# Kernel optimization log

Hardware: AMD Instinct MI355X
Metric: run time of the kernel (lower is better)

## Reference

```python
import jax, jax.numpy as jnp
import numpy as np

EPS = 1e-5  # BatchNorm2d default eps


def _conv3x3(x, w):
    # x: [B,C,H,W], w: [O,I,3,3], stride 1, 'same' padding (autopad k=3 -> p=1)
    return jax.lax.conv_general_dilated(
        x, w, window_strides=(1, 1), padding=((1, 1), (1, 1)),
        dimension_numbers=("NCHW", "OIHW", "NCHW"))


def _bn(x, g, b, m, v):
    # inference-mode BatchNorm2d with materialized running stats
    scale = (g / jnp.sqrt(v + EPS))[None, :, None, None]
    return (x - m[None, :, None, None]) * scale + b[None, :, None, None]


def _silu(x):
    return x * jax.nn.sigmoid(x)


def _pam(y, q_w, q_b, k_w, k_b, v_w, v_b, pam_gamma):
    # PAM_Module: full pixel-wise self-attention over N = H*W tokens
    B, C, H, W = y.shape
    N = H * W
    yf = y.reshape(B, C, N)
    # 1x1 convs expressed as channel matmuls; q_w: [C//8, C], v_w: [C, C]
    q = jnp.einsum("oc,bcn->bno", q_w, yf) + q_b                 # [B, N, C//8]
    k = jnp.einsum("oc,bcn->bon", k_w, yf) + k_b[None, :, None]  # [B, C//8, N]
    v = jnp.einsum("oc,bcn->bon", v_w, yf) + v_b[None, :, None]  # [B, C, N]
    energy = jnp.einsum("bno,bom->bnm", q, k)                    # [B, N, N]
    attn = jax.nn.softmax(energy, axis=-1)
    # torch: bmm(v, attn.permute(0,2,1)) -> out[b,c,n] = sum_m v[b,c,m] * attn[b,n,m]
    out = jnp.einsum("bcm,bnm->bcn", v, attn).reshape(B, C, H, W)
    return pam_gamma * out + y


def setup_inputs() -> dict:
    key = jax.random.key(0)
    ks = jax.random.split(key, 16)
    B, C1, C2, H, W = 4, 64, 64, 64, 64
    C_ = C2 // 2          # e = 0.5
    C8 = C2 // 8          # PAM q/k channels
    s = 0.05
    inp = {
        "x": jax.random.normal(ks[0], (B, C1, H, W), jnp.float32),
        # cv1: Conv(c1, c_, 3, 1)
        "cv1_w": jax.random.normal(ks[1], (C_, C1, 3, 3), jnp.float32) * s,
        "bn1_g": jax.random.uniform(ks[2], (C_,), jnp.float32, 0.5, 1.5),
        "bn1_b": jax.random.normal(ks[3], (C_,), jnp.float32) * s,
        "bn1_m": jax.random.normal(ks[4], (C_,), jnp.float32) * s,
        "bn1_v": jax.random.uniform(ks[5], (C_,), jnp.float32, 0.5, 1.5),
        # cv2: Conv(c_, c2, 3, 1)
        "cv2_w": jax.random.normal(ks[6], (C2, C_, 3, 3), jnp.float32) * s,
        "bn2_g": jax.random.uniform(ks[7], (C2,), jnp.float32, 0.5, 1.5),
        "bn2_b": jax.random.normal(ks[8], (C2,), jnp.float32) * s,
        "bn2_m": jax.random.normal(ks[9], (C2,), jnp.float32) * s,
        "bn2_v": jax.random.uniform(ks[10], (C2,), jnp.float32, 0.5, 1.5),
        # PAM 1x1 convs (flattened kernels) + biases + gamma
        "q_w": jax.random.normal(ks[11], (C8, C2), jnp.float32) * s,
        "q_b": jax.random.normal(ks[12], (C8,), jnp.float32) * s,
        "k_w": jax.random.normal(ks[13], (C8, C2), jnp.float32) * s,
        "k_b": jax.random.normal(ks[14], (C8,), jnp.float32) * s,
        "v_w": jax.random.normal(ks[15], (C2, C2), jnp.float32) * s,
        "v_b": jnp.zeros((C2,), jnp.float32),
        "pam_gamma": jnp.float32(0.5),  # torch inits 0 (identity); nonzero to exercise path
    }
    return inp


def reference(x, cv1_w, bn1_g, bn1_b, bn1_m, bn1_v,
              cv2_w, bn2_g, bn2_b, bn2_m, bn2_v,
              q_w, q_b, k_w, k_b, v_w, v_b, pam_gamma):
    y = _silu(_bn(_conv3x3(x, cv1_w), bn1_g, bn1_b, bn1_m, bn1_v))   # cv1
    y = _silu(_bn(_conv3x3(y, cv2_w), bn2_g, bn2_b, bn2_m, bn2_v))   # cv2
    # SAA: PAM applied twice on identical input and summed == 2 * PAM(y)
    att = 2.0 * _pam(y, q_w, q_b, k_w, k_b, v_w, v_b, pam_gamma)
    return x + att  # shortcut active (c1 == c2)
```

## Files before the change

### kernel.cpp

```cpp
#include <hip/hip_runtime.h>
#include <hip/hip_bf16.h>

#define NB 4
#define NN 4096

typedef short  bf16x8 __attribute__((ext_vector_type(8)));
typedef float  f32x4  __attribute__((ext_vector_type(4)));

static __device__ __forceinline__ ushort f2bf(float f) {
    unsigned u = __float_as_uint(f);
    u += 0x7fffu + ((u >> 16) & 1u);
    return (ushort)(u >> 16);
}

__global__ __launch_bounds__(256) void prep(
    const float* __restrict__ x, const float* __restrict__ w1, const float* __restrict__ w2,
    ushort* __restrict__ xt, ushort* __restrict__ W1r, ushort* __restrict__ W2r)
{
    const int tid = threadIdx.x;
    const int blk = blockIdx.x;
    if (blk < 256) {
        __shared__ float Ts[64][66];
        const int b = blk >> 6, n0 = (blk & 63) * 64;
        const int wv = tid >> 6, lane = tid & 63;
        #pragma unroll
        for (int i = 0; i < 16; ++i) {
            int ci = i * 4 + wv, nn = lane;
            Ts[ci][nn] = x[((size_t)b * 64 + ci) * NN + n0 + nn];
        }
        __syncthreads();
        #pragma unroll
        for (int i = 0; i < 16; ++i) {
            int nn = i * 4 + wv, ci = lane;
            xt[((size_t)b * NN + n0 + nn) * 64 + ci] = f2bf(Ts[ci][nn]);
        }
    } else if (blk < 258) {
        const int base = (blk - 256) * 9216;
        #pragma unroll
        for (int i = 0; i < 36; ++i) {
            int e = base + i * 256 + tid;
            int co = e / 576, k = e % 576, tap = k >> 6, ci = k & 63;
            W1r[e] = f2bf(w1[((size_t)co * 64 + ci) * 9 + tap]);
        }
    } else {
        const int base = (blk - 258) * 9216;
        #pragma unroll
        for (int i = 0; i < 36; ++i) {
            int e = base + i * 256 + tid;
            int co = e / 288, k = e % 288, tap = k >> 5, ci = k & 31;
            W2r[e] = f2bf(w2[((size_t)co * 32 + ci) * 9 + tap]);
        }
    }
}

__global__ __launch_bounds__(256) void conv1_mfma(
    const ushort* __restrict__ xt, const ushort* __restrict__ W1r,
    const float* __restrict__ bng, const float* __restrict__ bnb,
    const float* __restrict__ bnm, const float* __restrict__ bnv,
    ushort* __restrict__ y1t)
{
    __shared__ __align__(16) ushort As[32 * 600];
    __shared__ __align__(16) ushort Xs[24 * 66 * 8];

    const int tid = threadIdx.x;
    const int h = blockIdx.x, b = blockIdx.y;

    #pragma unroll
    for (int i = 0; i < 9; ++i) {
        int cid = i * 256 + tid;
        int row = cid / 72, off = cid % 72;
        *(uint4*)&As[row * 600 + off * 8] = *(const uint4*)(W1r + (size_t)cid * 8);
    }
    #pragma unroll
    for (int r = 0; r < 3; ++r) {
        int gh = h - 1 + r;
        #pragma unroll
        for (int i = 0; i < 2; ++i) {
            int cid = i * 256 + tid;
            int w_ = cid >> 3, cc = cid & 7;
            uint4 v = {0, 0, 0, 0};
            if ((unsigned)gh < 64u)
                v = *(const uint4*)(xt + ((size_t)(b * NN + gh * 64) * 64) + (size_t)cid * 8);
            *(uint4*)&Xs[((r * 8 + cc) * 66 + (w_ + 1)) * 8] = v;
        }
    }
    if (tid < 48) {
        int r = tid >> 4, q = tid & 15, cc = q >> 1, side = (q & 1) * 65;
        uint4 z = {0, 0, 0, 0};
        *(uint4*)&Xs[((r * 8 + cc) * 66 + side) * 8] = z;
    }
    __syncthreads();

    const int lane = tid & 63, wv = tid >> 6;
    const int quad = lane >> 4, l15 = lane & 15;
    const int ch = wv & 1, ph = wv >> 1;

    f32x4 acc[2] = {{0.f,0.f,0.f,0.f},{0.f,0.f,0.f,0.f}};
    #pragma unroll
    for (int kk = 0; kk < 18; ++kk) {
        const int tap = kk >> 1;
        const int dyr = tap / 3, dx = tap % 3;
        bf16x8 af = *(const bf16x8*)&As[(ch * 16 + l15) * 600 + kk * 32 + quad * 8];
        #pragma unroll
        for (int s = 0; s < 2; ++s) {
            int p = ph * 32 + s * 16 + l15;
            bf16x8 bf = *(const bf16x8*)&Xs[((dyr * 8 + (kk & 1) * 4 + quad) * 66 + p + dx) * 8];
            acc[s] = __builtin_amdgcn_mfma_f32_16x16x32_bf16(af, bf, acc[s], 0, 0, 0);
        }
    }

    const int cb = ch * 16 + quad * 4;
    float sc[4], bs[4];
    #pragma unroll
    for (int r = 0; r < 4; ++r) {
        int co = cb + r;
        sc[r] = bng[co] / sqrtf(bnv[co] + 1e-5f);
        bs[r] = bnb[co] - bnm[co] * sc[r];
    }
    #pragma unroll
    for (int s = 0; s < 2; ++s) {
        int p = ph * 32 + s * 16 + l15;
        ushort u4[4];
        #pragma unroll
        for (int r = 0; r < 4; ++r) {
            float pre = acc[s][r] * sc[r] + bs[r];
            u4[r] = f2bf(pre / (1.f + __expf(-pre)));
        }
        *(uint2*)&y1t[((size_t)(b * NN + h * 64 + p)) * 32 + cb] = *(uint2*)u4;
    }
}

__global__ __launch_bounds__(256) void conv2qkv(
    const ushort* __restrict__ y1t, const ushort* __restrict__ W2r,
    const float* __restrict__ bng, const float* __restrict__ bnb,
    const float* __restrict__ bnm, const float* __restrict__ bnv,
    const float* __restrict__ qw, const float* __restrict__ qb,
    const float* __restrict__ kw, const float* __restrict__ kb,
    const float* __restrict__ vw, const float* __restrict__ vb,
    float* __restrict__ y, ushort* __restrict__ q8,
    ushort* __restrict__ ko, ushort* __restrict__ vt)
{
    __shared__ __align__(16) ushort As[64 * 312];
    __shared__ __align__(16) ushort Xs[12 * 66 * 8];
    __shared__ __align__(16) ushort Yt[64 * 76];
    __shared__ __align__(16) ushort Wq[80 * 76];
    __shared__ float Bv[80];

    const int tid = threadIdx.x;
    const int h = blockIdx.x, b = blockIdx.y;

    #pragma unroll
    for (int i = 0; i < 9; ++i) {
        int cid = i * 256 + tid;
        int row = cid / 36, off = cid % 36;
        *(uint4*)&As[row * 312 + off * 8] = *(const uint4*)(W2r + (size_t)cid * 8);
    }
    #pragma unroll
    for (int r = 0; r < 3; ++r) {
        int gh = h - 1 + r;
        int cid = tid;
        int w_ = cid >> 2, cc = cid & 3;
        uint4 v = {0, 0, 0, 0};
        if ((unsigned)gh < 64u)
            v = *(const uint4*)(y1t + ((size_t)(b * NN + gh * 64) * 32) + (size_t)cid * 8);
        *(uint4*)&Xs[((r * 4 + cc) * 66 + (w_ + 1)) * 8] = v;
    }
    if (tid < 24) {
        int r = tid >> 3, q = tid & 7, cc = q >> 1, side = (q & 1) * 65;
        uint4 z = {0, 0, 0, 0};
        *(uint4*)&Xs[((r * 4 + cc) * 66 + side) * 8] = z;
    }
    for (int i = tid; i < 2560; i += 256) {
        int chw = i >> 5, c2 = (i & 31) * 2;
        const float* src = (chw < 8) ? (qw + chw * 64 + c2)
                         : (chw < 16) ? (kw + (chw - 8) * 64 + c2)
                         : (vw + (chw - 16) * 64 + c2);
        float2 v2 = *(const float2*)src;
        *(unsigned*)&Wq[chw * 76 + c2] = ((unsigned)f2bf(v2.y) << 16) | f2bf(v2.x);
    }
    if (tid < 80) Bv[tid] = (tid < 8) ? qb[tid] : (tid < 16) ? kb[tid - 8] : vb[tid - 16];
    __syncthreads();

    const int lane = tid & 63, wv = tid >> 6;
    const int quad = lane >> 4, l15 = lane & 15;

    f32x4 acc[4] = {{0.f,0.f,0.f,0.f},{0.f,0.f,0.f,0.f},{0.f,0.f,0.f,0.f},{0.f,0.f,0.f,0.f}};
    #pragma unroll
    for (int kk = 0; kk < 9; ++kk) {
        const int dyr = kk / 3, dx = kk % 3;
        bf16x8 af = *(const bf16x8*)&As[(wv * 16 + l15) * 312 + kk * 32 + quad * 8];
        #pragma unroll
        for (int s = 0; s < 4; ++s) {
            int p = s * 16 + l15;
            bf16x8 bf = *(const bf16x8*)&Xs[((dyr * 4 + quad) * 66 + p + dx) * 8];
            acc[s] = __builtin_amdgcn_mfma_f32_16x16x32_bf16(af, bf, acc[s], 0, 0, 0);
        }
    }

    const int cb = wv * 16 + quad * 4;
    float sc[4], bs[4];
    #pragma unroll
    for (int r = 0; r < 4; ++r) {
        int co = cb + r;
        sc[r] = bng[co] / sqrtf(bnv[co] + 1e-5f);
        bs[r] = bnb[co] - bnm[co] * sc[r];
    }
    #pragma unroll
    for (int s = 0; s < 4; ++s) {
        int p = s * 16 + l15;
        #pragma unroll
        for (int r = 0; r < 4; ++r) {
            float pre = acc[s][r] * sc[r] + bs[r];
            float res = pre / (1.f + __expf(-pre));
            y[((size_t)(b * 64 + cb + r)) * NN + h * 64 + p] = res;
            Yt[p * 76 + cb + r] = f2bf(res);
        }
    }
    __syncthreads();

    bf16x8 aY0 = *(const bf16x8*)&Yt[(wv * 16 + l15) * 76 + quad * 8];
    bf16x8 aY1 = *(const bf16x8*)&Yt[(wv * 16 + l15) * 76 + 32 + quad * 8];
    const int nbase = h * 64 + wv * 16 + quad * 4;
    const int vtile = h * 2 + (wv >> 1);
    const int vslot = quad * 8 + (wv & 1) * 4;
    #pragma unroll
    for (int cht = 0; cht < 5; ++cht) {
        bf16x8 bW0 = *(const bf16x8*)&Wq[(cht * 16 + l15) * 76 + quad * 8];
        bf16x8 bW1 = *(const bf16x8*)&Wq[(cht * 16 + l15) * 76 + 32 + quad * 8];
        f32x4 qa = {0.f, 0.f, 0.f, 0.f};
        qa = __builtin_amdgcn_mfma_f32_16x16x32_bf16(aY0, bW0, qa, 0, 0, 0);
        qa = __builtin_amdgcn_mfma_f32_16x16x32_bf16(aY1, bW1, qa, 0, 0, 0);
        const float bias = Bv[cht * 16 + l15];
        const int chn = cht * 16 + l15;
        if (cht == 0) {
            if (l15 < 8) {
                #pragma unroll
                for (int r = 0; r < 4; ++r)
                    q8[((size_t)b * NN + nbase + r) * 8 + chn] = f2bf(qa[r] + bias);
            } else {
                #pragma unroll
                for (int r = 0; r < 4; ++r)
                    ko[((size_t)b * NN + nbase + r) * 8 + (chn - 8)] = f2bf(qa[r] + bias);
            }
        } else {
            const int c = chn - 16;
            ushort u4[4];
            #pragma unroll
            for (int r = 0; r < 4; ++r) u4[r] = f2bf(qa[r] + bias);
            *(uint2*)&vt[(((size_t)(b * 128 + vtile)) * 64 + c) * 32 + vslot] = *(uint2*)u4;
        }
    }
}

__global__ __launch_bounds__(512, 4) void flash_pam(
    const ushort* __restrict__ q8,
    const ushort* __restrict__ k8,
    const ushort* __restrict__ vt,
    const float* __restrict__ y,
    const float* __restrict__ x,
    const float* __restrict__ gamma_p,
    float* __restrict__ out)
{
    __shared__ __align__(16) float Osum[4 * 2304];
    __shared__ float Lw[8][32];
    __shared__ float Ls[32];

    const int tid = threadIdx.x;
    const int bx = blockIdx.x;
    const int b  = bx >> 7;
    const int nt = bx & 127;
    const int n0 = nt * 32;

    const int lane = tid & 63, w = tid >> 6;
    const int quad = lane >> 4, l15 = lane & 15;

    const uint4 z4 = {0u, 0u, 0u, 0u};

    bf16x8 bQ[2];
    #pragma unroll
    for (int af = 0; af < 2; ++af) {
        uint4 qv = *(const uint4*)(q8 + ((size_t)b * NN + n0 + af * 16 + l15) * 8);
        uint4 sel = (quad == 0) ? qv : z4;
        bQ[af] = *(bf16x8*)&sel;
    }

    const ushort* kg = k8 + ((size_t)b * NN + w * 512) * 8;
    const ushort* vg = vt + ((size_t)(b * 128 + w * 16)) * 64 * 32;

    f32x4 acc[2][4] = {{{0.f,0.f,0.f,0.f},{0.f,0.f,0.f,0.f},{0.f,0.f,0.f,0.f},{0.f,0.f,0.f,0.f}},
                       {{0.f,0.f,0.f,0.f},{0.f,0.f,0.f,0.f},{0.f,0.f,0.f,0.f},{0.f,0.f,0.f,0.f}}};
    float lacc[2] = {0.f, 0.f};
    const f32x4 zf = {0.f, 0.f, 0.f, 0.f};

    #pragma unroll 2
    for (int t = 0; t < 16; ++t) {
        const int g = t * 32;
        uint4 k0r = *(const uint4*)(kg + (size_t)(g + l15) * 8);
        uint4 k1r = *(const uint4*)(kg + (size_t)(g + 16 + l15) * 8);
        uint4 k0s = (quad == 0) ? k0r : z4;
        uint4 k1s = (quad == 0) ? k1r : z4;
        bf16x8 aK0 = *(bf16x8*)&k0s;
        bf16x8 aK1 = *(bf16x8*)&k1s;

        bf16x8 vb_[4];
        #pragma unroll
        for (int ct = 0; ct < 4; ++ct)
            vb_[ct] = *(const bf16x8*)(vg + (size_t)t * 2048 + (ct * 16 + l15) * 32 + quad * 8);

        f32x4 s0[2], s1[2];
        #pragma unroll
        for (int af = 0; af < 2; ++af) {
            s0[af] = __builtin_amdgcn_mfma_f32_16x16x32_bf16(aK0, bQ[af], zf, 0, 0, 0);
            s1[af] = __builtin_amdgcn_mfma_f32_16x16x32_bf16(aK1, bQ[af], zf, 0, 0, 0);
        }

        bf16x8 pa[2];
        #pragma unroll
        for (int af = 0; af < 2; ++af) {
            union { ushort u[8]; bf16x8 v; } pk;
            #pragma unroll
            for (int r = 0; r < 4; ++r) {
                float e = __expf(s0[af][r]);
                lacc[af] += e;
                pk.u[r] = f2bf(e);
            }
            #pragma unroll
            for (int r = 0; r < 4; ++r) {
                float e = __expf(s1[af][r]);
                lacc[af] += e;
                pk.u[4 + r] = f2bf(e);
            }
            pa[af] = pk.v;
        }

        #pragma unroll
        for (int af = 0; af < 2; ++af)
            #pragma unroll
            for (int ct = 0; ct < 4; ++ct)
                acc[af][ct] = __builtin_amdgcn_mfma_f32_16x16x32_bf16(pa[af], vb_[ct], acc[af][ct], 0, 0, 0);
    }

    #pragma unroll
    for (int af = 0; af < 2; ++af) {
        lacc[af] += __shfl_xor(lacc[af], 16, 64);
        lacc[af] += __shfl_xor(lacc[af], 32, 64);
    }
    if (quad == 0) {
        Lw[w][l15]      = lacc[0];
        Lw[w][16 + l15] = lacc[1];
    }

    if (w >= 4) {
        #pragma unroll
        for (int af = 0; af < 2; ++af)
            #pragma unroll
            for (int ct = 0; ct < 4; ++ct)
                *(f32x4*)&Osum[(w - 4) * 2304 + (ct * 16 + l15) * 36 + af * 16 + quad * 4] = acc[af][ct];
    }
    __syncthreads();
    if (w < 4) {
        #pragma unroll
        for (int af = 0; af < 2; ++af)
            #pragma unroll
            for (int ct = 0; ct < 4; ++ct) {
                float* p = &Osum[w * 2304 + (ct * 16 + l15) * 36 + af * 16 + quad * 4];
                f32x4 v = *(const f32x4*)p;
                *(f32x4*)p = v + acc[af][ct];
            }
    }
    if (tid < 32) Ls[tid] = Lw[0][tid] + Lw[1][tid] + Lw[2][tid] + Lw[3][tid]
                          + Lw[4][tid] + Lw[5][tid] + Lw[6][tid] + Lw[7][tid];
    __syncthreads();

    {
        const int c = tid >> 3, nn = (tid & 7) * 4;
        f32x4 o = {0.f, 0.f, 0.f, 0.f};
        #pragma unroll
        for (int s = 0; s < 4; ++s)
            o += *(const f32x4*)&Osum[s * 2304 + c * 36 + nn];
        const float g2 = 2.f * gamma_p[0];
        const size_t idx = ((size_t)b * 64 + c) * NN + n0 + nn;
        f32x4 xv = *(const f32x4*)(x + idx);
        f32x4 yv = *(const f32x4*)(y + idx);
        f32x4 res;
        #pragma unroll
        for (int u = 0; u < 4; ++u)
            res[u] = xv[u] + 2.f * yv[u] + g2 * o[u] / Ls[nn + u];
        *(f32x4*)(out + idx) = res;
    }
}

extern "C" void kernel_launch(void* const* d_in, const int* in_sizes, int n_in,
                              void* d_out, int out_size, void* d_ws, size_t ws_size,
                              hipStream_t stream) {
    const float* x    = (const float*)d_in[0];
    const float* w1   = (const float*)d_in[1];
    const float* g1   = (const float*)d_in[2];
    const float* b1   = (const float*)d_in[3];
    const float* m1   = (const float*)d_in[4];
    const float* v1   = (const float*)d_in[5];
    const float* w2   = (const float*)d_in[6];
    const float* g2   = (const float*)d_in[7];
    const float* b2   = (const float*)d_in[8];
    const float* m2   = (const float*)d_in[9];
    const float* v2   = (const float*)d_in[10];
    const float* qw   = (const float*)d_in[11];
    const float* qb   = (const float*)d_in[12];
    const float* kw   = (const float*)d_in[13];
    const float* kb   = (const float*)d_in[14];
    const float* vw   = (const float*)d_in[15];
    const float* vb   = (const float*)d_in[16];
    const float* gam  = (const float*)d_in[17];
    float* outp = (float*)d_out;

    float* ws = (float*)d_ws;
    ushort* xt  = (ushort*)ws;
    float*  y   = ws + 524288;
    ushort* q8  = (ushort*)(ws + 1572864);
    ushort* kk  = (ushort*)(ws + 1703936);
    ushort* vv  = (ushort*)(ws + 1769472);
    float*  S   = ws + 2326528;
    ushort* y1t = (ushort*)S;
    ushort* W1r = (ushort*)(S + 262144);
    ushort* W2r = (ushort*)(S + 271360);

    prep<<<260, 256, 0, stream>>>(x, w1, w2, xt, W1r, W2r);
    conv1_mfma<<<dim3(64, NB), 256, 0, stream>>>(xt, W1r, g1, b1, m1, v1, y1t);
    conv2qkv<<<dim3(64, NB), 256, 0, stream>>>(y1t, W2r, g2, b2, m2, v2,
                                               qw, qb, kw, kb, vw, vb,
                                               y, q8, kk, vv);
    flash_pam<<<512, 512, 0, stream>>>(q8, kk, vv, y, x, gam, outp);
}
```

Baseline: 132.2 us.

## Double flash_pam query tile to 64 and store residual y as bf16

Each flash_pam block now handles 64 query positions instead of 32, so every K/V fragment loaded is reused across four query sub-tiles, halving the K/V global traffic per query. The grid drops to 256 blocks, launch bounds are relaxed to 2 blocks per SM, and the shared reduction buffer is enlarged. The intermediate y tensor is also written and read as bf16 rather than fp32, reducing memory traffic but adding rounding to the residual term. Fewer blocks and higher register pressure may hurt occupancy and latency hiding.

```diff
diff --git a/kernel.cpp b/kernel.cpp
--- a/kernel.cpp
+++ b/kernel.cpp
@@ -12,6 +12,8 @@
     u += 0x7fffu + ((u >> 16) & 1u);
     return (ushort)(u >> 16);
 }
+static __device__ __forceinline__ float bflo(unsigned w) { return __uint_as_float(w << 16); }
+static __device__ __forceinline__ float bfhi(unsigned w) { return __uint_as_float(w & 0xffff0000u); }
 
 __global__ __launch_bounds__(256) void prep(
     const float* __restrict__ x, const float* __restrict__ w1, const float* __restrict__ w2,
@@ -137,7 +139,7 @@
     const float* __restrict__ qw, const float* __restrict__ qb,
     const float* __restrict__ kw, const float* __restrict__ kb,
     const float* __restrict__ vw, const float* __restrict__ vb,
-    float* __restrict__ y, ushort* __restrict__ q8,
+    ushort* __restrict__ yb, ushort* __restrict__ q8,
     ushort* __restrict__ ko, ushort* __restrict__ vt)
 {
     __shared__ __align__(16) ushort As[64 * 312];
@@ -212,8 +214,9 @@
         for (int r = 0; r < 4; ++r) {
             float pre = acc[s][r] * sc[r] + bs[r];
             float res = pre / (1.f + __expf(-pre));
-            y[((size_t)(b * 64 + cb + r)) * NN + h * 64 + p] = res;
-            Yt[p * 76 + cb + r] = f2bf(res);
+            ushort rb = f2bf(res);
+            yb[((size_t)(b * 64 + cb + r)) * NN + h * 64 + p] = rb;
+            Yt[p * 76 + cb + r] = rb;
         }
     }
     __syncthreads();
@@ -252,33 +255,33 @@
     }
 }
 
-__global__ __launch_bounds__(512, 4) void flash_pam(
+__global__ __launch_bounds__(512, 2) void flash_pam(
     const ushort* __restrict__ q8,
     const ushort* __restrict__ k8,
     const ushort* __restrict__ vt,
-    const float* __restrict__ y,
+    const ushort* __restrict__ yb,
     const float* __restrict__ x,
     const float* __restrict__ gamma_p,
     float* __restrict__ out)
 {
-    __shared__ __align__(16) float Osum[4 * 2304];
-    __shared__ float Lw[8][32];
-    __shared__ float Ls[32];
+    __shared__ __align__(16) float Osum[4 * 64 * 68];
+    __shared__ float Lw[8][64];
+    __shared__ float Ls[64];
 
     const int tid = threadIdx.x;
     const int bx = blockIdx.x;
-    const int b  = bx >> 7;
-    const int nt = bx & 127;
-    const int n0 = nt * 32;
+    const int b  = bx >> 6;
+    const int nt = bx & 63;
+    const int n0 = nt * 64;
 
     const int lane = tid & 63, w = tid >> 6;
     const int quad = lane >> 4, l15 = lane & 15;
 
     const uint4 z4 = {0u, 0u, 0u, 0u};
 
-    bf16x8 bQ[2];
-    #pragma unroll
-    for (int af = 0; af < 2; ++af) {
+    bf16x8 bQ[4];
+    #pragma unroll
+    for (int af = 0; af < 4; ++af) {
         uint4 qv = *(const uint4*)(q8 + ((size_t)b * NN + n0 + af * 16 + l15) * 8);
         uint4 sel = (quad == 0) ? qv : z4;
         bQ[af] = *(bf16x8*)&sel;
@@ -287,12 +290,14 @@
     const ushort* kg = k8 + ((size_t)b * NN + w * 512) * 8;
     const ushort* vg = vt + ((size_t)(b * 128 + w * 16)) * 64 * 32;
 
-    f32x4 acc[2][4] = {{{0.f,0.f,0.f,0.f},{0.f,0.f,0.f,0.f},{0.f,0.f,0.f,0.f},{0.f,0.f,0.f,0.f}},
-                       {{0.f,0.f,0.f,0.f},{0.f,0.f,0.f,0.f},{0.f,0.f,0.f,0.f},{0.f,0.f,0.f,0.f}}};
-    float lacc[2] = {0.f, 0.f};
+    f32x4 acc[4][4];
+    #pragma unroll
+    for (int af = 0; af < 4; ++af)
+        #pragma unroll
+        for (int ct = 0; ct < 4; ++ct) acc[af][ct] = {0.f, 0.f, 0.f, 0.f};
+    float lacc[4] = {0.f, 0.f, 0.f, 0.f};
     const f32x4 zf = {0.f, 0.f, 0.f, 0.f};
 
-    #pragma unroll 2
     for (int t = 0; t < 16; ++t) {
         const int g = t * 32;
         uint4 k0r = *(const uint4*)(kg + (size_t)(g + l15) * 8);
@@ -307,86 +312,81 @@
         for (int ct = 0; ct < 4; ++ct)
             vb_[ct] = *(const bf16x8*)(vg + (size_t)t * 2048 + (ct * 16 + l15) * 32 + quad * 8);
 
-        f32x4 s0[2], s1[2];
-        #pragma unroll
-        for (int af = 0; af < 2; ++af) {
-            s0[af] = __builtin_amdgcn_mfma_f32_16x16x32_bf16(aK0, bQ[af], zf, 0, 0, 0);
-            s1[af] = __builtin_amdgcn_mfma_f32_16x16x32_bf16(aK1, bQ[af], zf, 0, 0, 0);
-        }
-
-        bf16x8 pa[2];
-        #pragma unroll
-        for (int af = 0; af < 2; ++af) {
+        #pragma unroll
+        for (int af = 0; af < 4; ++af) {
+            f32x4 s0 = __builtin_amdgcn_mfma_f32_16x16x32_bf16(aK0, bQ[af], zf, 0, 0, 0);
+            f32x4 s1 = __builtin_amdgcn_mfma_f32_16x16x32_bf16(aK1, bQ[af], zf, 0, 0, 0);
             union { ushort u[8]; bf16x8 v; } pk;
             #pragma unroll
             for (int r = 0; r < 4; ++r) {
-                float e = __expf(s0[af][r]);
+                float e = __expf(s0[r]);
                 lacc[af] += e;
                 pk.u[r] = f2bf(e);
             }
             #pragma unroll
             for (int r = 0; r < 4; ++r) {
-                float e = __expf(s1[af][r]);
+                float e = __expf(s1[r]);
                 lacc[af] += e;
                 pk.u[4 + r] = f2bf(e);
             }
-            pa[af] = pk.v;
-        }
-
-        #pragma unroll
-        for (int af = 0; af < 2; ++af)
             #pragma unroll
             for (int ct = 0; ct < 4; ++ct)
-                acc[af][ct] = __builtin_amdgcn_mfma_f32_16x16x32_bf16(pa[af], vb_[ct], acc[af][ct], 0, 0, 0);
-    }
-
-    #pragma unroll
-    for (int af = 0; af < 2; ++af) {
+                acc[af][ct] = __builtin_amdgcn_mfma_f32_16x16x32_bf16(pk.v, vb_[ct], acc[af][ct], 0, 0, 0);
+        }
+    }
+
+    #pragma unroll
+    for (int af = 0; af < 4; ++af) {
         lacc[af] += __shfl_xor(lacc[af], 16, 64);
         lacc[af] += __shfl_xor(lacc[af], 32, 64);
     }
     if (quad == 0) {
-        Lw[w][l15]      = lacc[0];
-        Lw[w][16 + l15] = lacc[1];
+        #pragma unroll
+        for (int af = 0; af < 4; ++af) Lw[w][af * 16 + l15] = lacc[af];
     }
 
     if (w >= 4) {
         #pragma unroll
-        for (int af = 0; af < 2; ++af)
+        for (int af = 0; af < 4; ++af)
             #pragma unroll
             for (int ct = 0; ct < 4; ++ct)
-                *(f32x4*)&Osum[(w - 4) * 2304 + (ct * 16 + l15) * 36 + af * 16 + quad * 4] = acc[af][ct];
+                *(f32x4*)&Osum[((w - 4) * 64 + ct * 16 + l15) * 68 + af * 16 + quad * 4] = acc[af][ct];
     }
     __syncthreads();
     if (w < 4) {
         #pragma unroll
-        for (int af = 0; af < 2; ++af)
+        for (int af = 0; af < 4; ++af)
             #pragma unroll
             for (int ct = 0; ct < 4; ++ct) {
-                float* p = &Osum[w * 2304 + (ct * 16 + l15) * 36 + af * 16 + quad * 4];
+                float* p = &Osum[(w * 64 + ct * 16 + l15) * 68 + af * 16 + quad * 4];
                 f32x4 v = *(const f32x4*)p;
                 *(f32x4*)p = v + acc[af][ct];
             }
     }
-    if (tid < 32) Ls[tid] = Lw[0][tid] + Lw[1][tid] + Lw[2][tid] + Lw[3][tid]
+    if (tid < 64) Ls[tid] = Lw[0][tid] + Lw[1][tid] + Lw[2][tid] + Lw[3][tid]
                           + Lw[4][tid] + Lw[5][tid] + Lw[6][tid] + Lw[7][tid];
     __syncthreads();
 
     {
-        const int c = tid >> 3, nn = (tid & 7) * 4;
-        f32x4 o = {0.f, 0.f, 0.f, 0.f};
-        #pragma unroll
-        for (int s = 0; s < 4; ++s)
-            o += *(const f32x4*)&Osum[s * 2304 + c * 36 + nn];
+        const int c = tid >> 3, nb = (tid & 7) * 8;
         const float g2 = 2.f * gamma_p[0];
-        const size_t idx = ((size_t)b * 64 + c) * NN + n0 + nn;
-        f32x4 xv = *(const f32x4*)(x + idx);
-        f32x4 yv = *(const f32x4*)(y + idx);
-        f32x4 res;
-        #pragma unroll
-        for (int u = 0; u < 4; ++u)
-            res[u] = xv[u] + 2.f * yv[u] + g2 * o[u] / Ls[nn + u];
-        *(f32x4*)(out + idx) = res;
+        #pragma unroll
+        for (int hh = 0; hh < 2; ++hh) {
+            const int nn = nb + hh * 4;
+            f32x4 o = {0.f, 0.f, 0.f, 0.f};
+            #pragma unroll
+            for (int s = 0; s < 4; ++s)
+                o += *(const f32x4*)&Osum[(s * 64 + c) * 68 + nn];
+            const size_t idx = ((size_t)b * 64 + c) * NN + n0 + nn;
+            f32x4 xv = *(const f32x4*)(x + idx);
+            uint2 yv2 = *(const uint2*)(yb + idx);
+            float yf[4] = { bflo(yv2.x), bfhi(yv2.x), bflo(yv2.y), bfhi(yv2.y) };
+            f32x4 res;
+            #pragma unroll
+            for (int u = 0; u < 4; ++u)
+                res[u] = xv[u] + 2.f * yf[u] + g2 * o[u] / Ls[nn + u];
+            *(f32x4*)(out + idx) = res;
+        }
     }
 }
 
@@ -415,7 +415,7 @@
 
     float* ws = (float*)d_ws;
     ushort* xt  = (ushort*)ws;
-    float*  y   = ws + 524288;
+    ushort* yb  = (ushort*)(ws + 524288);
     ushort* q8  = (ushort*)(ws + 1572864);
     ushort* kk  = (ushort*)(ws + 1703936);
     ushort* vv  = (ushort*)(ws + 1769472);
@@ -428,6 +428,6 @@
     conv1_mfma<<<dim3(64, NB), 256, 0, stream>>>(xt, W1r, g1, b1, m1, v1, y1t);
     conv2qkv<<<dim3(64, NB), 256, 0, stream>>>(y1t, W2r, g2, b2, m2, v2,
                                                qw, qb, kw, kb, vw, vb,
-                                               y, q8, kk, vv);
-    flash_pam<<<512, 512, 0, stream>>>(q8, kk, vv, y, x, gam, outp);
-}
+                                               yb, q8, kk, vv);
+    flash_pam<<<256, 512, 0, stream>>>(q8, kk, vv, yb, x, gam, outp);
+}
```

Result: slower. 136.5 us (+3.3%).
